# Performance work log

Hardware: AMD Instinct MI355X
Metric: run time of the kernel (lower is better)

Reference implementation:

```python
import jax, jax.numpy as jnp
import numpy as np

NUM_HEADS = 12


def setup_inputs() -> dict:
    key = jax.random.key(0)
    ks = jax.random.split(key, 6)
    B, T, D = 512, 128, 768  # batch, seq (<= CONTEXT_LENGTH=128), d_model
    d_in, d_out = D, D
    s_in = 1.0 / np.sqrt(d_in)
    s_out = 1.0 / np.sqrt(d_out)
    return {
        "x": jax.random.normal(ks[0], (B, T, d_in), dtype=jnp.float32),
        "Wq": jax.random.uniform(ks[1], (d_in, d_out), jnp.float32, -s_in, s_in),
        "Wk": jax.random.uniform(ks[2], (d_in, d_out), jnp.float32, -s_in, s_in),
        "Wv": jax.random.uniform(ks[3], (d_in, d_out), jnp.float32, -s_in, s_in),
        "Wo": jax.random.uniform(ks[4], (d_out, d_out), jnp.float32, -s_out, s_out),
        "bo": jax.random.uniform(ks[5], (d_out,), jnp.float32, -s_out, s_out),
    }


def reference(x, Wq, Wk, Wv, Wo, bo):
    B, T, _ = x.shape
    H = NUM_HEADS
    hd = Wq.shape[1] // H
    # projections -> [b, h, t, hd]
    q = jnp.einsum("btd,de->bte", x, Wq).reshape(B, T, H, hd).transpose(0, 2, 1, 3)
    k = jnp.einsum("btd,de->bte", x, Wk).reshape(B, T, H, hd).transpose(0, 2, 1, 3)
    v = jnp.einsum("btd,de->bte", x, Wv).reshape(B, T, H, hd).transpose(0, 2, 1, 3)
    scores = jnp.einsum("bhqd,bhkd->bhqk", q, k)
    causal = jnp.tril(jnp.ones((T, T), dtype=bool))  # True = keep
    scores = jnp.where(causal, scores, -jnp.inf)
    attn = jax.nn.softmax(scores / jnp.sqrt(jnp.float32(hd)), axis=-1)
    # dropout is identity in eval mode
    ctx = jnp.einsum("bhqk,bhkd->bhqd", attn, v)
    ctx = ctx.transpose(0, 2, 1, 3).reshape(B, T, H * hd)
    return jnp.einsum("btd,de->bte", ctx, Wo) + bo
```

## Files before the change

### kernel.cpp

```cpp
#include <hip/hip_runtime.h>
#include <hip/hip_bf16.h>
#include <cstdint>
#include <math.h>


typedef __bf16 bf16;
typedef __bf16 bf16x8 __attribute__((ext_vector_type(8)));
typedef float f32x4 __attribute__((ext_vector_type(4)));

#define MFMA16(a, b, c) __builtin_amdgcn_mfma_f32_16x16x32_bf16((a), (b), (c), 0, 0, 0)

#define GLD_LDS16(gp, lp)                                                       \
  __builtin_amdgcn_global_load_lds(                                             \
      (const __attribute__((address_space(1))) void*)(gp),                      \
      (__attribute__((address_space(3))) void*)(lp), 16, 0, 0)

__global__ __launch_bounds__(256) void cast_x_bf16(const float* __restrict__ in,
                                                   bf16* __restrict__ out, int n) {
  int i = (blockIdx.x * 256 + threadIdx.x) * 4;
  if (i < n) {
    float4 v = *(const float4*)(in + i);
    bf16 o[4] = {(bf16)v.x, (bf16)v.y, (bf16)v.z, (bf16)v.w};
    *(uint2*)(out + i) = *(const uint2*)o;
  }
}

__global__ __launch_bounds__(256) void transpose_cast_w(const float* __restrict__ W,
                                                        bf16* __restrict__ Out) {
  __shared__ float t[32][33];
  int bx = blockIdx.x * 32;
  int by = blockIdx.y * 32;
  int tx = threadIdx.x, ty = threadIdx.y;
  for (int i = 0; i < 32; i += 8)
    t[ty + i][tx] = W[(size_t)(bx + ty + i) * 768 + by + tx];
  __syncthreads();
  for (int i = 0; i < 32; i += 8)
    Out[(size_t)(by + ty + i) * 768 + bx + tx] = (bf16)t[tx][ty + i];
}

template <bool OUT_F32>
__global__ __launch_bounds__(512, 2) void gemm256(
    const bf16* __restrict__ A, int lda, const bf16* __restrict__ Bt, int ldb,
    void* __restrict__ Cout, int ldc, const float* __restrict__ bias, int K,
    int ntn) {
  __shared__ bf16 smem[2 * 32768];

  const int tid = threadIdx.x;
  const int lane = tid & 63;
  const int w = tid >> 6;

  const int nwg = gridDim.x;
  const int wg = (blockIdx.x & 7) * (nwg >> 3) + (blockIdx.x >> 3);
  const int m0 = (wg / ntn) * 256;
  const int n0 = (wg % ntn) * 256;

  const int r0 = tid >> 2;
  const int c0 = ((((tid & 3) * 16) ^ (((tid >> 3) & 3) << 4)) >> 1);
  const bf16* As0 = A + (size_t)(m0 + r0) * lda + c0;
  const bf16* As1 = As0 + (size_t)128 * lda;
  const bf16* Bs0 = Bt + (size_t)(n0 + r0) * ldb + c0;
  const bf16* Bs1 = Bs0 + (size_t)128 * ldb;

  const int lm = lane & 15;
  const int kqs = ((lane >> 4) * 8) ^ (((lm >> 1) & 3) << 3);
  const int wm = (w & 1) * 128;
  const int wn = (w >> 1) * 64;
  const bf16* pA = smem + (wm + lm) * 32 + kqs;
  const bf16* pB = smem + 16384 + (wn + lm) * 32 + kqs;

  f32x4 acc[8][4];
#pragma unroll
  for (int i = 0; i < 8; ++i)
#pragma unroll
    for (int j = 0; j < 4; ++j) acc[i][j] = (f32x4){0.f, 0.f, 0.f, 0.f};

  bf16x8 af[4], bfr[4];

  const int NT = K >> 6;
  const int NH = NT >> 1;

  auto SA = [&](int t, int kh) {
    const int ko = t * 64 + kh * 32;
    const int lo = (t & 1) * 32768 + kh * 8192;
    GLD_LDS16(As0 + ko, smem + lo + w * 512);
    GLD_LDS16(As1 + ko, smem + lo + 4096 + w * 512);
  };
  auto SB = [&](int t, int kh) {
    const int ko = t * 64 + kh * 32;
    const int lo = (t & 1) * 32768 + 16384 + kh * 8192;
    GLD_LDS16(Bs0 + ko, smem + lo + w * 512);
    GLD_LDS16(Bs1 + ko, smem + lo + 4096 + w * 512);
  };
  auto RD = [&](int buf, int kh, int h, bool lb) {
    const bf16* a = pA + buf * 32768 + kh * 8192 + h * 2048;
#pragma unroll
    for (int j = 0; j < 4; ++j) af[j] = *(const bf16x8*)(a + j * 512);
    if (lb) {
      const bf16* b = pB + buf * 32768 + kh * 8192;
#pragma unroll
      for (int j = 0; j < 4; ++j) bfr[j] = *(const bf16x8*)(b + j * 512);
    }
  };
  auto BAR = [&](int vm) {
    __builtin_amdgcn_sched_barrier(0);
    if (vm == 6) asm volatile("s_waitcnt vmcnt(6)" ::: "memory");
    else if (vm == 0) asm volatile("s_waitcnt vmcnt(0)" ::: "memory");
    __builtin_amdgcn_s_barrier();
    asm volatile("s_waitcnt lgkmcnt(0)" ::: "memory");
    __builtin_amdgcn_sched_barrier(0);
  };
  auto MM = [&](int h) {
    __builtin_amdgcn_s_setprio(1);
#pragma unroll
    for (int j = 0; j < 4; ++j)
#pragma unroll
      for (int n = 0; n < 4; ++n)
        acc[h * 4 + j][n] = MFMA16(af[j], bfr[n], acc[h * 4 + j][n]);
    __builtin_amdgcn_s_setprio(0);
  };

  SB(0, 0); SA(0, 0); SB(0, 1); SA(0, 1);
  asm volatile("s_waitcnt vmcnt(4)" ::: "memory");
  SB(1, 0); SA(1, 0); SB(1, 1);
  asm volatile("s_waitcnt vmcnt(6)" ::: "memory");
  __builtin_amdgcn_s_barrier();
  __builtin_amdgcn_sched_barrier(0);

  for (int i = 0; i < NH - 1; ++i) {
    const int t1 = 2 * i + 1, t2 = 2 * i + 2, t3 = 2 * i + 3;
    RD(0, 0, 0, true);  SA(t1, 1); BAR(-1); MM(0);
    RD(0, 0, 1, false); SB(t2, 0); BAR(-1); MM(1);
    RD(0, 1, 0, true);  SA(t2, 0); BAR(-1); MM(0);
    RD(0, 1, 1, false); SB(t2, 1); BAR(6);  MM(1);
    RD(1, 0, 0, true);  SA(t2, 1); BAR(-1); MM(0);
    RD(1, 0, 1, false); SB(t3, 0); BAR(-1); MM(1);
    RD(1, 1, 0, true);  SA(t3, 0); BAR(-1); MM(0);
    RD(1, 1, 1, false); SB(t3, 1); BAR(6);  MM(1);
  }
  RD(0, 0, 0, true);  SA(NT - 1, 1); BAR(-1); MM(0);
  RD(0, 0, 1, false);                BAR(-1); MM(1);
  RD(0, 1, 0, true);                 BAR(-1); MM(0);
  RD(0, 1, 1, false);                BAR(0);  MM(1);
  RD(1, 0, 0, true);                 BAR(-1); MM(0);
  RD(1, 0, 1, false);                BAR(-1); MM(1);
  RD(1, 1, 0, true);                 BAR(-1); MM(0);
  RD(1, 1, 1, false);                BAR(-1); MM(1);

  __syncthreads();

  const int lr = (lane >> 4) * 4;
  if constexpr (!OUT_F32) {
    const unsigned exw = (unsigned)(lane >> 4) << 5;
#pragma unroll
    for (int mi = 0; mi < 8; ++mi)
#pragma unroll
      for (int ni = 0; ni < 4; ++ni) {
        const int colb = (wn + ni * 16 + lm) * 2;
#pragma unroll
        for (int r = 0; r < 4; ++r) {
          const unsigned ad = (unsigned)(wm + mi * 16 + lr + r) * 512 + colb;
          *(bf16*)((char*)smem + (ad ^ exw)) = (bf16)acc[mi][ni][r];
        }
      }
    __syncthreads();
    const unsigned exr = (unsigned)((tid >> 7) & 3) << 5;
#pragma unroll
    for (int s = 0; s < 16; ++s) {
      const int e = s * 4096 + tid * 8;
      const int row = e >> 8, col = e & 255;
      uint4 v = *(const uint4*)((char*)smem + (((unsigned)row * 512 + col * 2) ^ exr));
      *(uint4*)((bf16*)Cout + (size_t)(m0 + row) * ldc + n0 + col) = v;
    }
  } else {
    const unsigned exw = (unsigned)(lane >> 4) << 6;
#pragma unroll
    for (int h = 0; h < 2; ++h) {
      __syncthreads();
      if ((w & 1) == h) {
#pragma unroll
        for (int mi = 0; mi < 8; ++mi)
#pragma unroll
          for (int ni = 0; ni < 4; ++ni) {
            const int colb = (wn + ni * 16 + lm) * 4;
#pragma unroll
            for (int r = 0; r < 4; ++r) {
              const unsigned ad = (unsigned)(mi * 16 + lr + r) * 1024 + colb;
              *(float*)((char*)smem + (ad ^ exw)) = acc[mi][ni][r];
            }
          }
      }
      __syncthreads();
#pragma unroll
      for (int s = 0; s < 16; ++s) {
        const int row = s * 8 + w;
        const int col = (lane & 63) * 4;
        const unsigned xr = (unsigned)((row >> 2) & 3) << 6;
        float4 v = *(const float4*)((char*)smem + (((unsigned)row * 1024 + col * 4) ^ xr));
        float4 bb = *(const float4*)(bias + n0 + col);
        v.x += bb.x; v.y += bb.y; v.z += bb.z; v.w += bb.w;
        *(float4*)((float*)Cout + (size_t)(m0 + h * 128 + row) * ldc + n0 + col) = v;
      }
    }
  }
}

__global__ __launch_bounds__(256, 3) void attn_kernel(const bf16* __restrict__ qkv,
                                                      bf16* __restrict__ ctx) {
  constexpr int LDQ = 2304;
  constexpr int SKS = 72;
  constexpr int SPS = 136;
  __shared__ bf16 smem[26112];
  bf16* sK = smem;
  bf16* sP = smem;
  bf16* sVt = smem + 17408;

  const int bh = (blockIdx.x & 7) * 768 + (blockIdx.x >> 3);
  const int b = bh / 12, h = bh % 12;
  const bf16* Qg = qkv + (size_t)b * 128 * LDQ + h * 64;
  const bf16* Kg = Qg + 768;
  const bf16* Vg = Qg + 1536;

  const int tid = threadIdx.x;
  const int lane = tid & 63;
  const int w = tid >> 6;
  const int lm = lane & 15;
  const int kq = (lane >> 4) * 8;
  const int lr = (lane >> 4) * 4;

  bf16x8 aq[2][2];
#pragma unroll
  for (int mi = 0; mi < 2; ++mi)
#pragma unroll
    for (int kk2 = 0; kk2 < 2; ++kk2)
      aq[mi][kk2] = *(const bf16x8*)(Qg + (size_t)(w * 32 + mi * 16 + lm) * LDQ +
                                     kk2 * 32 + kq);

  {
    int row = tid >> 1, half = tid & 1;
    const uint4* ksrc = (const uint4*)(Kg + (size_t)row * LDQ + half * 32);
    const uint4* vsrc = (const uint4*)(Vg + (size_t)row * LDQ + half * 32);
    uint4* kdst = (uint4*)(sK + row * SKS + half * 32);
    uint4 vt[4];
    for (int i = 0; i < 4; ++i) {
      kdst[i] = ksrc[i];
      vt[i] = vsrc[i];
    }
    const bf16* tp = (const bf16*)vt;
    for (int d = 0; d < 32; ++d) sVt[(half * 32 + d) * SPS + row] = tp[d];
  }
  __syncthreads();

  f32x4 sacc[2][8];
  for (int i = 0; i < 2; ++i)
    for (int j = 0; j < 8; ++j) sacc[i][j] = (f32x4){0.f, 0.f, 0.f, 0.f};
  for (int kk2 = 0; kk2 < 2; ++kk2) {
    bf16x8 bk[8];
    for (int ni = 0; ni < 8; ++ni)
      bk[ni] = *(const bf16x8*)(sK + (ni * 16 + lm) * SKS + kk2 * 32 + kq);
    for (int mi = 0; mi < 2; ++mi)
      for (int ni = 0; ni < 8; ++ni)
        sacc[mi][ni] = MFMA16(aq[mi][kk2], bk[ni], sacc[mi][ni]);
  }

  float inv[2][4];
  for (int mi = 0; mi < 2; ++mi) {
    for (int r = 0; r < 4; ++r) {
      int row = w * 32 + mi * 16 + lr + r;
      float vals[8];
      float mx = -INFINITY;
      for (int ni = 0; ni < 8; ++ni) {
        int col = ni * 16 + lm;
        float v = sacc[mi][ni][r] * 0.125f;
        if (col > row) v = -INFINITY;
        vals[ni] = v;
        mx = fmaxf(mx, v);
      }
      for (int off = 1; off < 16; off <<= 1) mx = fmaxf(mx, __shfl_xor(mx, off, 64));
      float sum = 0.f;
      for (int ni = 0; ni < 8; ++ni) {
        float p = __expf(vals[ni] - mx);
        vals[ni] = p;
        sum += p;
      }
      for (int off = 1; off < 16; off <<= 1) sum += __shfl_xor(sum, off, 64);
      inv[mi][r] = 1.f / sum;
      for (int ni = 0; ni < 8; ++ni) sacc[mi][ni][r] = vals[ni];
    }
  }
  __syncthreads();

  for (int mi = 0; mi < 2; ++mi)
    for (int ni = 0; ni < 8; ++ni)
      for (int r = 0; r < 4; ++r) {
        int row = w * 32 + mi * 16 + lr + r;
        int col = ni * 16 + lm;
        sP[row * SPS + col] = (bf16)sacc[mi][ni][r];
      }
  __syncthreads();

  f32x4 oacc[2][4];
  for (int i = 0; i < 2; ++i)
    for (int j = 0; j < 4; ++j) oacc[i][j] = (f32x4){0.f, 0.f, 0.f, 0.f};
  for (int kk = 0; kk < 128; kk += 32) {
    bf16x8 ap[2], bv[4];
    for (int mi = 0; mi < 2; ++mi)
      ap[mi] = *(const bf16x8*)(sP + (w * 32 + mi * 16 + lm) * SPS + kk + kq);
    for (int ci = 0; ci < 4; ++ci)
      bv[ci] = *(const bf16x8*)(sVt + (ci * 16 + lm) * SPS + kk + kq);
    for (int mi = 0; mi < 2; ++mi)
      for (int ci = 0; ci < 4; ++ci)
        oacc[mi][ci] = MFMA16(ap[mi], bv[ci], oacc[mi][ci]);
  }

  bf16* Cg = ctx + (size_t)b * 128 * LDQ + h * 64;
  for (int mi = 0; mi < 2; ++mi)
    for (int ci = 0; ci < 4; ++ci)
      for (int r = 0; r < 4; ++r) {
        int row = w * 32 + mi * 16 + lr + r;
        int col = ci * 16 + lm;
        Cg[(size_t)row * LDQ + col] = (bf16)(oacc[mi][ci][r] * inv[mi][r]);
      }
}

extern "C" void kernel_launch(void* const* d_in, const int* in_sizes, int n_in,
                              void* d_out, int out_size, void* d_ws, size_t ws_size,
                              hipStream_t stream) {
  const float* x = (const float*)d_in[0];
  const float* Wq = (const float*)d_in[1];
  const float* Wk = (const float*)d_in[2];
  const float* Wv = (const float*)d_in[3];
  const float* Wo = (const float*)d_in[4];
  const float* bo = (const float*)d_in[5];
  float* out = (float*)d_out;

  constexpr int M = 512 * 128;
  constexpr int D = 768;
  constexpr size_t XB_BYTES = (size_t)M * D * 2;
  constexpr size_t WQKV_BYTES = (size_t)3 * D * D * 2;
  constexpr size_t WOT_BYTES = (size_t)D * D * 2;

  char* ws = (char*)d_ws;
  bf16* xb = (bf16*)ws;
  bf16* wqkv = (bf16*)(ws + XB_BYTES);
  bf16* wot = (bf16*)(ws + XB_BYTES + WQKV_BYTES);
  bf16* qkv = (bf16*)(ws + XB_BYTES + WQKV_BYTES + WOT_BYTES);

  cast_x_bf16<<<(M * D) / 1024, 256, 0, stream>>>(x, xb, M * D);
  dim3 tb(32, 8);
  transpose_cast_w<<<dim3(24, 24), tb, 0, stream>>>(Wq, wqkv);
  transpose_cast_w<<<dim3(24, 24), tb, 0, stream>>>(Wk, wqkv + 768 * 768);
  transpose_cast_w<<<dim3(24, 24), tb, 0, stream>>>(Wv, wqkv + 2 * 768 * 768);
  transpose_cast_w<<<dim3(24, 24), tb, 0, stream>>>(Wo, wot);
  gemm256<false><<<dim3(2304), 512, 0, stream>>>(xb, 768, wqkv, 768, qkv, 2304,
                                                 nullptr, 768, 9);
  attn_kernel<<<512 * 12, 256, 0, stream>>>(qkv, qkv);
  gemm256<true><<<dim3(768), 512, 0, stream>>>(qkv, 2304, wot, 768, out, 768,
                                               bo, 768, 3);
}
```

Baseline: 767.0 us.

## Shrink GEMM tiles to 128x256 with BK=32 triple-buffered LDS pipeline

The bf16 GEMM moves from 256x256 tiles with a double-buffered BK=64 schedule to 128x256 tiles with a three-stage BK=32 ring buffer. Each K step now issues one A load and two B loads. This cuts LDS use per block to 72 KiB and halves the accumulator registers, and launch bounds ask for 4 blocks per CU instead of 2. It trades less operand reuse per tile and more barriers per K for higher occupancy and twice as many blocks in the grid.

```diff
diff --git a/kernel.cpp b/kernel.cpp
--- a/kernel.cpp
+++ b/kernel.cpp
@@ -39,11 +39,11 @@
 }
 
 template <bool OUT_F32>
-__global__ __launch_bounds__(512, 2) void gemm256(
+__global__ __launch_bounds__(512, 4) void gemm_bk32(
     const bf16* __restrict__ A, int lda, const bf16* __restrict__ Bt, int ldb,
     void* __restrict__ Cout, int ldc, const float* __restrict__ bias, int K,
     int ntn) {
-  __shared__ bf16 smem[2 * 32768];
+  __shared__ bf16 smem[3 * 12288];
 
   const int tid = threadIdx.x;
   const int lane = tid & 63;
@@ -51,154 +51,128 @@
 
   const int nwg = gridDim.x;
   const int wg = (blockIdx.x & 7) * (nwg >> 3) + (blockIdx.x >> 3);
-  const int m0 = (wg / ntn) * 256;
+  const int m0 = (wg / ntn) * 128;
   const int n0 = (wg % ntn) * 256;
 
   const int r0 = tid >> 2;
   const int c0 = ((((tid & 3) * 16) ^ (((tid >> 3) & 3) << 4)) >> 1);
   const bf16* As0 = A + (size_t)(m0 + r0) * lda + c0;
-  const bf16* As1 = As0 + (size_t)128 * lda;
   const bf16* Bs0 = Bt + (size_t)(n0 + r0) * ldb + c0;
   const bf16* Bs1 = Bs0 + (size_t)128 * ldb;
 
   const int lm = lane & 15;
   const int kqs = ((lane >> 4) * 8) ^ (((lm >> 1) & 3) << 3);
-  const int wm = (w & 1) * 128;
+  const int wm = (w & 1) * 64;
   const int wn = (w >> 1) * 64;
   const bf16* pA = smem + (wm + lm) * 32 + kqs;
-  const bf16* pB = smem + 16384 + (wn + lm) * 32 + kqs;
-
-  f32x4 acc[8][4];
-#pragma unroll
-  for (int i = 0; i < 8; ++i)
+  const bf16* pB = smem + 4096 + (wn + lm) * 32 + kqs;
+
+  f32x4 acc[4][4];
+#pragma unroll
+  for (int i = 0; i < 4; ++i)
 #pragma unroll
     for (int j = 0; j < 4; ++j) acc[i][j] = (f32x4){0.f, 0.f, 0.f, 0.f};
 
-  bf16x8 af[4], bfr[4];
-
-  const int NT = K >> 6;
-  const int NH = NT >> 1;
-
-  auto SA = [&](int t, int kh) {
-    const int ko = t * 64 + kh * 32;
-    const int lo = (t & 1) * 32768 + kh * 8192;
-    GLD_LDS16(As0 + ko, smem + lo + w * 512);
-    GLD_LDS16(As1 + ko, smem + lo + 4096 + w * 512);
+  const int NT = K >> 5;
+
+  auto STAGE = [&](int t, int sb) {
+    const int k0 = t * 32;
+    bf16* base = smem + sb * 12288;
+    GLD_LDS16(As0 + k0, base + w * 512);
+    GLD_LDS16(Bs0 + k0, base + 4096 + w * 512);
+    GLD_LDS16(Bs1 + k0, base + 8192 + w * 512);
   };
-  auto SB = [&](int t, int kh) {
-    const int ko = t * 64 + kh * 32;
-    const int lo = (t & 1) * 32768 + 16384 + kh * 8192;
-    GLD_LDS16(Bs0 + ko, smem + lo + w * 512);
-    GLD_LDS16(Bs1 + ko, smem + lo + 4096 + w * 512);
-  };
-  auto RD = [&](int buf, int kh, int h, bool lb) {
-    const bf16* a = pA + buf * 32768 + kh * 8192 + h * 2048;
-#pragma unroll
-    for (int j = 0; j < 4; ++j) af[j] = *(const bf16x8*)(a + j * 512);
-    if (lb) {
-      const bf16* b = pB + buf * 32768 + kh * 8192;
-#pragma unroll
-      for (int j = 0; j < 4; ++j) bfr[j] = *(const bf16x8*)(b + j * 512);
-    }
-  };
-  auto BAR = [&](int vm) {
+
+  STAGE(0, 0);
+  STAGE(1, 1);
+  asm volatile("s_waitcnt vmcnt(3)" ::: "memory");
+  __builtin_amdgcn_s_barrier();
+  __builtin_amdgcn_sched_barrier(0);
+
+  int rb = 0, sb = 2;
+  for (int t = 0; t < NT; ++t) {
+    const bf16* a = pA + rb * 12288;
+    const bf16* b = pB + rb * 12288;
+    bf16x8 af[4], bfr[4];
+#pragma unroll
+    for (int mi = 0; mi < 4; ++mi) af[mi] = *(const bf16x8*)(a + mi * 512);
+#pragma unroll
+    for (int ni = 0; ni < 4; ++ni) bfr[ni] = *(const bf16x8*)(b + ni * 512);
+
+    if (t + 2 < NT) STAGE(t + 2, sb);
     __builtin_amdgcn_sched_barrier(0);
-    if (vm == 6) asm volatile("s_waitcnt vmcnt(6)" ::: "memory");
-    else if (vm == 0) asm volatile("s_waitcnt vmcnt(0)" ::: "memory");
+    if (t + 2 < NT)
+      asm volatile("s_waitcnt vmcnt(3)" ::: "memory");
+    else if (t + 2 == NT)
+      asm volatile("s_waitcnt vmcnt(0)" ::: "memory");
     __builtin_amdgcn_s_barrier();
     asm volatile("s_waitcnt lgkmcnt(0)" ::: "memory");
     __builtin_amdgcn_sched_barrier(0);
-  };
-  auto MM = [&](int h) {
+
     __builtin_amdgcn_s_setprio(1);
 #pragma unroll
-    for (int j = 0; j < 4; ++j)
-#pragma unroll
-      for (int n = 0; n < 4; ++n)
-        acc[h * 4 + j][n] = MFMA16(af[j], bfr[n], acc[h * 4 + j][n]);
+    for (int mi = 0; mi < 4; ++mi)
+#pragma unroll
+      for (int ni = 0; ni < 4; ++ni)
+        acc[mi][ni] = MFMA16(af[mi], bfr[ni], acc[mi][ni]);
     __builtin_amdgcn_s_setprio(0);
-  };
-
-  SB(0, 0); SA(0, 0); SB(0, 1); SA(0, 1);
-  asm volatile("s_waitcnt vmcnt(4)" ::: "memory");
-  SB(1, 0); SA(1, 0); SB(1, 1);
-  asm volatile("s_waitcnt vmcnt(6)" ::: "memory");
-  __builtin_amdgcn_s_barrier();
-  __builtin_amdgcn_sched_barrier(0);
-
-  for (int i = 0; i < NH - 1; ++i) {
-    const int t1 = 2 * i + 1, t2 = 2 * i + 2, t3 = 2 * i + 3;
-    RD(0, 0, 0, true);  SA(t1, 1); BAR(-1); MM(0);
-    RD(0, 0, 1, false); SB(t2, 0); BAR(-1); MM(1);
-    RD(0, 1, 0, true);  SA(t2, 0); BAR(-1); MM(0);
-    RD(0, 1, 1, false); SB(t2, 1); BAR(6);  MM(1);
-    RD(1, 0, 0, true);  SA(t2, 1); BAR(-1); MM(0);
-    RD(1, 0, 1, false); SB(t3, 0); BAR(-1); MM(1);
-    RD(1, 1, 0, true);  SA(t3, 0); BAR(-1); MM(0);
-    RD(1, 1, 1, false); SB(t3, 1); BAR(6);  MM(1);
-  }
-  RD(0, 0, 0, true);  SA(NT - 1, 1); BAR(-1); MM(0);
-  RD(0, 0, 1, false);                BAR(-1); MM(1);
-  RD(0, 1, 0, true);                 BAR(-1); MM(0);
-  RD(0, 1, 1, false);                BAR(0);  MM(1);
-  RD(1, 0, 0, true);                 BAR(-1); MM(0);
-  RD(1, 0, 1, false);                BAR(-1); MM(1);
-  RD(1, 1, 0, true);                 BAR(-1); MM(0);
-  RD(1, 1, 1, false);                BAR(-1); MM(1);
+
+    rb = rb == 2 ? 0 : rb + 1;
+    sb = sb == 2 ? 0 : sb + 1;
+  }
 
   __syncthreads();
 
   const int lr = (lane >> 4) * 4;
   if constexpr (!OUT_F32) {
-    const unsigned exw = (unsigned)(lane >> 4) << 5;
-#pragma unroll
-    for (int mi = 0; mi < 8; ++mi)
+#pragma unroll
+    for (int mi = 0; mi < 4; ++mi)
 #pragma unroll
       for (int ni = 0; ni < 4; ++ni) {
         const int colb = (wn + ni * 16 + lm) * 2;
 #pragma unroll
         for (int r = 0; r < 4; ++r) {
-          const unsigned ad = (unsigned)(wm + mi * 16 + lr + r) * 512 + colb;
-          *(bf16*)((char*)smem + (ad ^ exw)) = (bf16)acc[mi][ni][r];
+          const int row = wm + mi * 16 + lr + r;
+          const unsigned ad = ((unsigned)row * 512 + colb) ^ (((row >> 2) & 3) << 5);
+          *(bf16*)((char*)smem + ad) = (bf16)acc[mi][ni][r];
         }
       }
     __syncthreads();
-    const unsigned exr = (unsigned)((tid >> 7) & 3) << 5;
-#pragma unroll
-    for (int s = 0; s < 16; ++s) {
-      const int e = s * 4096 + tid * 8;
-      const int row = e >> 8, col = e & 255;
-      uint4 v = *(const uint4*)((char*)smem + (((unsigned)row * 512 + col * 2) ^ exr));
+#pragma unroll
+    for (int s = 0; s < 8; ++s) {
+      const unsigned e = s * 8192 + tid * 16;
+      const int row = e >> 9, col = (e & 511) >> 1;
+      uint4 v = *(const uint4*)((char*)smem + (e ^ (((row >> 2) & 3) << 5)));
       *(uint4*)((bf16*)Cout + (size_t)(m0 + row) * ldc + n0 + col) = v;
     }
   } else {
-    const unsigned exw = (unsigned)(lane >> 4) << 6;
 #pragma unroll
     for (int h = 0; h < 2; ++h) {
       __syncthreads();
       if ((w & 1) == h) {
 #pragma unroll
-        for (int mi = 0; mi < 8; ++mi)
+        for (int mi = 0; mi < 4; ++mi)
 #pragma unroll
           for (int ni = 0; ni < 4; ++ni) {
             const int colb = (wn + ni * 16 + lm) * 4;
 #pragma unroll
             for (int r = 0; r < 4; ++r) {
-              const unsigned ad = (unsigned)(mi * 16 + lr + r) * 1024 + colb;
-              *(float*)((char*)smem + (ad ^ exw)) = acc[mi][ni][r];
+              const int row = mi * 16 + lr + r;
+              const unsigned ad =
+                  ((unsigned)row * 1024 + colb) ^ (((row >> 2) & 3) << 6);
+              *(float*)((char*)smem + ad) = acc[mi][ni][r];
             }
           }
       }
       __syncthreads();
 #pragma unroll
-      for (int s = 0; s < 16; ++s) {
-        const int row = s * 8 + w;
-        const int col = (lane & 63) * 4;
-        const unsigned xr = (unsigned)((row >> 2) & 3) << 6;
-        float4 v = *(const float4*)((char*)smem + (((unsigned)row * 1024 + col * 4) ^ xr));
+      for (int s = 0; s < 8; ++s) {
+        const unsigned e = s * 8192 + tid * 16;
+        const int row = e >> 10, col = (e & 1023) >> 2;
+        float4 v = *(const float4*)((char*)smem + (e ^ (((row >> 2) & 3) << 6)));
         float4 bb = *(const float4*)(bias + n0 + col);
         v.x += bb.x; v.y += bb.y; v.z += bb.z; v.w += bb.w;
-        *(float4*)((float*)Cout + (size_t)(m0 + h * 128 + row) * ldc + n0 + col) = v;
+        *(float4*)((float*)Cout + (size_t)(m0 + h * 64 + row) * ldc + n0 + col) = v;
       }
     }
   }
@@ -351,9 +325,9 @@
   transpose_cast_w<<<dim3(24, 24), tb, 0, stream>>>(Wk, wqkv + 768 * 768);
   transpose_cast_w<<<dim3(24, 24), tb, 0, stream>>>(Wv, wqkv + 2 * 768 * 768);
   transpose_cast_w<<<dim3(24, 24), tb, 0, stream>>>(Wo, wot);
-  gemm256<false><<<dim3(2304), 512, 0, stream>>>(xb, 768, wqkv, 768, qkv, 2304,
-                                                 nullptr, 768, 9);
+  gemm_bk32<false><<<dim3(4608), 512, 0, stream>>>(xb, 768, wqkv, 768, qkv,
+                                                   2304, nullptr, 768, 9);
   attn_kernel<<<512 * 12, 256, 0, stream>>>(qkv, qkv);
-  gemm256<true><<<dim3(768), 512, 0, stream>>>(qkv, 2304, wot, 768, out, 768,
-                                               bo, 768, 3);
-}
+  gemm_bk32<true><<<dim3(1536), 512, 0, stream>>>(qkv, 2304, wot, 768, out, 768,
+                                                  bo, 768, 3);
+}
```

Result: no change. 781.7 us (+1.9%).

## Double-buffer LDS fragment registers to overlap LDS reads with MFMA in GEMM

Applied to the files above, without the earlier changes.

The GEMM main loop now uses two register sets each for the A and B fragments, so the LDS reads for the next sub-step are issued before the MFMAs of the current one. It also drops the lgkmcnt(0) wait that followed each barrier. The global-to-LDS prefetch order and the vmcnt thresholds are rearranged to match, with a new vmcnt(4) case in the tail. The aim is to hide LDS latency behind matrix math, at the cost of more VGPRs and more delicate wait-count correctness.

```diff
diff --git a/kernel.cpp b/kernel.cpp
--- a/kernel.cpp
+++ b/kernel.cpp
@@ -74,7 +74,7 @@
 #pragma unroll
     for (int j = 0; j < 4; ++j) acc[i][j] = (f32x4){0.f, 0.f, 0.f, 0.f};
 
-  bf16x8 af[4], bfr[4];
+  bf16x8 afX[4], afY[4], bfU[4], bfV[4];
 
   const int NT = K >> 6;
   const int NH = NT >> 1;
@@ -91,60 +91,64 @@
     GLD_LDS16(Bs0 + ko, smem + lo + w * 512);
     GLD_LDS16(Bs1 + ko, smem + lo + 4096 + w * 512);
   };
-  auto RD = [&](int buf, int kh, int h, bool lb) {
+  auto rdA = [&](bf16x8* d, int buf, int kh, int h) {
     const bf16* a = pA + buf * 32768 + kh * 8192 + h * 2048;
 #pragma unroll
-    for (int j = 0; j < 4; ++j) af[j] = *(const bf16x8*)(a + j * 512);
-    if (lb) {
-      const bf16* b = pB + buf * 32768 + kh * 8192;
-#pragma unroll
-      for (int j = 0; j < 4; ++j) bfr[j] = *(const bf16x8*)(b + j * 512);
-    }
+    for (int j = 0; j < 4; ++j) d[j] = *(const bf16x8*)(a + j * 512);
+  };
+  auto rdB = [&](bf16x8* d, int buf, int kh) {
+    const bf16* b = pB + buf * 32768 + kh * 8192;
+#pragma unroll
+    for (int j = 0; j < 4; ++j) d[j] = *(const bf16x8*)(b + j * 512);
   };
   auto BAR = [&](int vm) {
     __builtin_amdgcn_sched_barrier(0);
     if (vm == 6) asm volatile("s_waitcnt vmcnt(6)" ::: "memory");
+    else if (vm == 4) asm volatile("s_waitcnt vmcnt(4)" ::: "memory");
     else if (vm == 0) asm volatile("s_waitcnt vmcnt(0)" ::: "memory");
     __builtin_amdgcn_s_barrier();
-    asm volatile("s_waitcnt lgkmcnt(0)" ::: "memory");
     __builtin_amdgcn_sched_barrier(0);
   };
-  auto MM = [&](int h) {
+  auto MM = [&](bf16x8* a, bf16x8* b, int h) {
     __builtin_amdgcn_s_setprio(1);
 #pragma unroll
     for (int j = 0; j < 4; ++j)
 #pragma unroll
       for (int n = 0; n < 4; ++n)
-        acc[h * 4 + j][n] = MFMA16(af[j], bfr[n], acc[h * 4 + j][n]);
+        acc[h * 4 + j][n] = MFMA16(a[j], b[n], acc[h * 4 + j][n]);
     __builtin_amdgcn_s_setprio(0);
   };
 
-  SB(0, 0); SA(0, 0); SB(0, 1); SA(0, 1);
-  asm volatile("s_waitcnt vmcnt(4)" ::: "memory");
-  SB(1, 0); SA(1, 0); SB(1, 1);
+  SA(0, 0); SB(0, 0); SA(0, 1); SB(0, 1);
+  SA(1, 0); SB(1, 0); SA(1, 1);
   asm volatile("s_waitcnt vmcnt(6)" ::: "memory");
   __builtin_amdgcn_s_barrier();
   __builtin_amdgcn_sched_barrier(0);
+  rdA(afX, 0, 0, 0);
+  rdB(bfU, 0, 0);
 
   for (int i = 0; i < NH - 1; ++i) {
     const int t1 = 2 * i + 1, t2 = 2 * i + 2, t3 = 2 * i + 3;
-    RD(0, 0, 0, true);  SA(t1, 1); BAR(-1); MM(0);
-    RD(0, 0, 1, false); SB(t2, 0); BAR(-1); MM(1);
-    RD(0, 1, 0, true);  SA(t2, 0); BAR(-1); MM(0);
-    RD(0, 1, 1, false); SB(t2, 1); BAR(6);  MM(1);
-    RD(1, 0, 0, true);  SA(t2, 1); BAR(-1); MM(0);
-    RD(1, 0, 1, false); SB(t3, 0); BAR(-1); MM(1);
-    RD(1, 1, 0, true);  SA(t3, 0); BAR(-1); MM(0);
-    RD(1, 1, 1, false); SB(t3, 1); BAR(6);  MM(1);
-  }
-  RD(0, 0, 0, true);  SA(NT - 1, 1); BAR(-1); MM(0);
-  RD(0, 0, 1, false);                BAR(-1); MM(1);
-  RD(0, 1, 0, true);                 BAR(-1); MM(0);
-  RD(0, 1, 1, false);                BAR(0);  MM(1);
-  RD(1, 0, 0, true);                 BAR(-1); MM(0);
-  RD(1, 0, 1, false);                BAR(-1); MM(1);
-  RD(1, 1, 0, true);                 BAR(-1); MM(0);
-  RD(1, 1, 1, false);                BAR(-1); MM(1);
+     rdA(afY, 0, 0, 1);                   SB(t1, 1); BAR(-1); MM(afX, bfU, 0);
+     rdA(afX, 0, 1, 0); rdB(bfV, 0, 1);   SA(t2, 0); BAR(6);  MM(afY, bfU, 1);
+     rdA(afY, 0, 1, 1);                   SB(t2, 0); BAR(-1); MM(afX, bfV, 0);
+     rdA(afX, 1, 0, 0); rdB(bfU, 1, 0);   SA(t2, 1); BAR(6);  MM(afY, bfV, 1);
+     rdA(afY, 1, 0, 1);                   SB(t2, 1); BAR(-1); MM(afX, bfU, 0);
+     rdA(afX, 1, 1, 0); rdB(bfV, 1, 1);   SA(t3, 0); BAR(6);  MM(afY, bfU, 1);
+     rdA(afY, 1, 1, 1);                   SB(t3, 0); BAR(-1); MM(afX, bfV, 0);
+     rdA(afX, 0, 0, 0); rdB(bfU, 0, 0);   SA(t3, 1); BAR(6);  MM(afY, bfV, 1);
+  }
+  {
+    const int t1 = NT - 1;
+     rdA(afY, 0, 0, 1);                   SB(t1, 1); BAR(-1); MM(afX, bfU, 0);
+     rdA(afX, 0, 1, 0); rdB(bfV, 0, 1);              BAR(4);  MM(afY, bfU, 1);
+     rdA(afY, 0, 1, 1);                              BAR(-1); MM(afX, bfV, 0);
+     rdA(afX, 1, 0, 0); rdB(bfU, 1, 0);              BAR(0);  MM(afY, bfV, 1);
+     rdA(afY, 1, 0, 1);                              BAR(-1); MM(afX, bfU, 0);
+     rdA(afX, 1, 1, 0); rdB(bfV, 1, 1);              BAR(-1); MM(afY, bfU, 1);
+     rdA(afY, 1, 1, 1);                              BAR(-1); MM(afX, bfV, 0);
+                                                     BAR(-1); MM(afY, bfV, 1);
+  }
 
   __syncthreads();
 
```

Result: no change. 779.5 us (+1.6%).
